# Performance work log

Hardware: AMD Instinct MI355X
Metric: run time of the kernel (lower is better)

## Reference

```python
import jax, jax.numpy as jnp
import numpy as np

B, S, V, D = 8, 1024, 8192, 256
MAX_POS = 1024


def _positional_encoding(position, d_model):
    pos = np.arange(position)[:, None].astype(np.float32)
    i = np.arange(d_model)[None, :].astype(np.float32)
    angle_rads = pos / np.power(10000.0, 2.0 * np.floor(i / 2.0) / np.float32(d_model))
    angle_rads[:, 0::2] = np.sin(angle_rads[:, 0::2])
    angle_rads[:, 1::2] = np.cos(angle_rads[:, 1::2])
    return jnp.asarray(angle_rads[None, ...], dtype=jnp.float32)  # [1, position, d_model]


def setup_inputs() -> dict:
    key = jax.random.key(0)
    k1, k2 = jax.random.split(key)
    x = jax.random.randint(k1, (B, S, V), 0, 2, dtype=jnp.int32)  # multi-hot mask
    emb_table = jax.random.normal(k2, (V, D), dtype=jnp.float32) * 0.02
    pos_enc = _positional_encoding(MAX_POS, D)
    return {"x": x, "emb_table": emb_table, "pos_enc": pos_enc}


def reference(x, emb_table, pos_enc):
    # Multi-hot embedding-bag: sum_v x[b,s,v] * emb_table[v,:]  (dense O(V) reduction,
    # faithful to get_emb's full-vocab embed * mask + reduce_sum)
    seq_len = x.shape[1]
    d_model = emb_table.shape[1]
    xf = x.astype(jnp.float32)
    emb = jnp.einsum('bsv,vd->bsd', xf, emb_table)
    emb = emb * jnp.sqrt(jnp.float32(d_model))
    # positional encoding gated by whether the position has any active token
    any_tok = (jnp.sum(x, axis=-1) > 0).astype(jnp.float32)[..., None]  # [B,S,1]
    out = emb + pos_enc[:, :seq_len, :] * any_tok
    # dropout is identity in eval mode; num_layers = 0 -> no encoder layers
    return out
```

## Files before the change

kernel.cpp:

```cpp
#include <hip/hip_runtime.h>


#define M_TOT 8192
#define K_TOT 8192
#define D_DIM 256
#define KSPLIT 8
#define KCHUNK (K_TOT / KSPLIT)
#define BK 32

typedef short  short8  __attribute__((ext_vector_type(8)));
typedef float  floatx4 __attribute__((ext_vector_type(4)));
typedef int    intx4   __attribute__((ext_vector_type(4)));

union S8U { intx4 i; short8 s; };

#define WS_RS_OFF (4u * 1024u * 1024u)

__device__ __forceinline__ unsigned int bf16_rne(float f) {
    unsigned int u = __float_as_uint(f);
    u += 0x7fffu + ((u >> 16) & 1u);
    return u >> 16;
}

__global__ __launch_bounds__(256) void zero_kernel(float* __restrict__ out, int* __restrict__ rs) {
    int b = blockIdx.x;
    if (b < 2048) {
        floatx4 z = {0.f, 0.f, 0.f, 0.f};
        *(floatx4*)(out + ((size_t)b * 256 + threadIdx.x) * 4) = z;
    } else {
        intx4 z = {0, 0, 0, 0};
        *(intx4*)(rs + ((size_t)(b - 2048) * 256 + threadIdx.x) * 4) = z;
    }
}

__global__ __launch_bounds__(256) void prep_kernel(const float* __restrict__ emb,
                                                   unsigned short* __restrict__ wsBf) {
    int gid = blockIdx.x * 256 + threadIdx.x;
    int l  = gid & 63;
    int kb = (gid >> 6) & 255;
    int c  = gid >> 14;
    int d  = c * 16 + (l & 15);
    int v0 = kb * 32 + (l >> 4) * 8;
    const float* src = emb + (size_t)v0 * D_DIM + d;
    intx4 q;
#pragma unroll
    for (int p = 0; p < 4; ++p) {
        unsigned int u0 = bf16_rne(src[(size_t)(2 * p) * D_DIM] * 16.0f);
        unsigned int u1 = bf16_rne(src[(size_t)(2 * p + 1) * D_DIM] * 16.0f);
        q[p] = (int)(u0 | (u1 << 16));
    }
    *(intx4*)(wsBf + (size_t)gid * 8) = q;
}

__global__ __launch_bounds__(256) void gemm_kernel(const int* __restrict__ x,
                                                   const unsigned short* __restrict__ wsBf,
                                                   float* __restrict__ out,
                                                   int* __restrict__ rs) {
    const int m0   = blockIdx.x * 64;
    const int kbeg = blockIdx.y * KCHUNK;
    const int t    = threadIdx.x;
    const int wave = t >> 6, lane = t & 63;
    const int quad = lane >> 4, rl = lane & 15;
    const int n0   = wave * 64;

    floatx4 acc[4][4];
#pragma unroll
    for (int i = 0; i < 4; ++i)
#pragma unroll
        for (int j = 0; j < 4; ++j) acc[i][j] = (floatx4){0.f, 0.f, 0.f, 0.f};

    int rp[4] = {0, 0, 0, 0};

    const int* abase = x + (size_t)(m0 + rl) * K_TOT + kbeg + quad * 8;
    const unsigned short* bbase = wsBf + ((size_t)(n0 >> 4) * 256) * 512 + (size_t)lane * 8;

#pragma unroll 2
    for (int kk = 0; kk < KCHUNK; kk += BK) {
        const int kb = (kbeg + kk) >> 5;

        short8 bf[4];
#pragma unroll
        for (int j = 0; j < 4; ++j)
            bf[j] = ((const S8U*)(bbase + ((size_t)j * 256 + kb) * 512))->s;

        short8 af[4];
#pragma unroll
        for (int i = 0; i < 4; ++i) {
            const int* p = abase + (size_t)(i * 16) * K_TOT + kk;
            intx4 a0 = *(const intx4*)p;
            intx4 a1 = *(const intx4*)(p + 4);
            int p0 = a0[0] | (a0[1] << 16);
            int p1 = a0[2] | (a0[3] << 16);
            int p2 = a1[0] | (a1[1] << 16);
            int p3 = a1[2] | (a1[3] << 16);
            if (wave == 0) rp[i] += p0 + p1 + p2 + p3;
            S8U u;
            u.i[0] = p0 * 0x3F80;
            u.i[1] = p1 * 0x3F80;
            u.i[2] = p2 * 0x3F80;
            u.i[3] = p3 * 0x3F80;
            af[i] = u.s;
        }

#pragma unroll
        for (int i = 0; i < 4; ++i)
#pragma unroll
            for (int j = 0; j < 4; ++j)
                acc[i][j] = __builtin_amdgcn_mfma_f32_16x16x32_bf16(af[i], bf[j], acc[i][j], 0, 0, 0);
    }

    if (wave == 0) {
#pragma unroll
        for (int i = 0; i < 4; ++i) {
            int cnt = (rp[i] & 0xFFFF) + (rp[i] >> 16);
            cnt += __shfl_xor(cnt, 16);
            cnt += __shfl_xor(cnt, 32);
            if (quad == 0) atomicAdd(&rs[m0 + i * 16 + rl], cnt);
        }
    }

#pragma unroll
    for (int i = 0; i < 4; ++i) {
#pragma unroll
        for (int j = 0; j < 4; ++j) {
            int col = n0 + j * 16 + rl;
#pragma unroll
            for (int r = 0; r < 4; ++r) {
                int row = m0 + i * 16 + quad * 4 + r;
                unsafeAtomicAdd(&out[(size_t)row * D_DIM + col], acc[i][j][r]);
            }
        }
    }
}

__global__ __launch_bounds__(256) void epi_kernel(float* __restrict__ out,
                                                  const float* __restrict__ pos,
                                                  const int* __restrict__ rs) {
    int gid  = blockIdx.x * 256 + threadIdx.x;
    int base = gid * 4;
    int row  = base >> 8;
    int col  = base & 255;
    if (rs[row] > 0) {
        int s = row & 1023;
        floatx4 o = *(floatx4*)(out + base);
        floatx4 p = *(const floatx4*)(pos + (size_t)s * D_DIM + col);
        o += p;
        *(floatx4*)(out + base) = o;
    }
}

extern "C" void kernel_launch(void* const* d_in, const int* in_sizes, int n_in,
                              void* d_out, int out_size, void* d_ws, size_t ws_size,
                              hipStream_t stream) {
    const int*   x   = (const int*)d_in[0];
    const float* emb = (const float*)d_in[1];
    const float* pos = (const float*)d_in[2];
    float*       out = (float*)d_out;

    unsigned short* wsBf = (unsigned short*)d_ws;
    int*            rs   = (int*)((char*)d_ws + WS_RS_OFF);

    zero_kernel<<<dim3(2056), dim3(256), 0, stream>>>(out, rs);
    prep_kernel<<<dim3(1024), dim3(256), 0, stream>>>(emb, wsBf);
    gemm_kernel<<<dim3(128, KSPLIT), dim3(256), 0, stream>>>(x, wsBf, out, rs);
    epi_kernel<<<dim3(2048), dim3(256), 0, stream>>>(out, pos, rs);
}
```

Before: 475.4 us.

## Stage A tiles via async LDS loads, replace atomic split-K with partial-buffer reduction

The GEMM now stages the int32 mask tiles into double-buffered, XOR-swizzled LDS using global_load_lds, so the next tile's global load overlaps the current tile's MFMAs. The tile is reshaped to 32 rows by 256 columns with K split 4 ways. Each split writes plain stores to its own partial buffer instead of atomically adding into a zeroed output. A fused reduce kernel then sums the partials, applies the row-count gate and adds the positional encoding, which removes the zero kernel and the float atomics. The cost is 32 MB of extra partial traffic and more re-reads of the B tiles, since each block now covers fewer rows.

```diff
diff --git a/kernel.cpp b/kernel.cpp
--- a/kernel.cpp
+++ b/kernel.cpp
@@ -1,12 +1,15 @@
 #include <hip/hip_runtime.h>
+#include <stdint.h>
 
 
-#define M_TOT 8192
 #define K_TOT 8192
 #define D_DIM 256
-#define KSPLIT 8
+#define KSPLIT 4
 #define KCHUNK (K_TOT / KSPLIT)
-#define BK 32
+#define BK 64
+#define TROWS 32
+#define NTILES (KCHUNK / BK)
+#define PART_STRIDE (8192u * 256u)
 
 typedef short  short8  __attribute__((ext_vector_type(8)));
 typedef float  floatx4 __attribute__((ext_vector_type(4)));
@@ -14,7 +17,8 @@
 
 union S8U { intx4 i; short8 s; };
 
-#define WS_RS_OFF (4u * 1024u * 1024u)
+#define WS_PART_OFF (4u * 1024u * 1024u)
+#define WS_RS_OFF   (36u * 1024u * 1024u)
 
 __device__ __forceinline__ unsigned int bf16_rne(float f) {
     unsigned int u = __float_as_uint(f);
@@ -22,15 +26,10 @@
     return u >> 16;
 }
 
-__global__ __launch_bounds__(256) void zero_kernel(float* __restrict__ out, int* __restrict__ rs) {
-    int b = blockIdx.x;
-    if (b < 2048) {
-        floatx4 z = {0.f, 0.f, 0.f, 0.f};
-        *(floatx4*)(out + ((size_t)b * 256 + threadIdx.x) * 4) = z;
-    } else {
-        intx4 z = {0, 0, 0, 0};
-        *(intx4*)(rs + ((size_t)(b - 2048) * 256 + threadIdx.x) * 4) = z;
-    }
+__device__ __forceinline__ void load_lds16(const int* g, int* l) {
+    __builtin_amdgcn_global_load_lds((const __attribute__((address_space(1))) unsigned int*)g,
+                                     (__attribute__((address_space(3))) unsigned int*)l,
+                                     16, 0, 0);
 }
 
 __global__ __launch_bounds__(256) void prep_kernel(const float* __restrict__ emb,
@@ -54,99 +53,127 @@
 
 __global__ __launch_bounds__(256) void gemm_kernel(const int* __restrict__ x,
                                                    const unsigned short* __restrict__ wsBf,
-                                                   float* __restrict__ out,
-                                                   int* __restrict__ rs) {
-    const int m0   = blockIdx.x * 64;
-    const int kbeg = blockIdx.y * KCHUNK;
+                                                   float* __restrict__ part,
+                                                   int* __restrict__ rsp) {
+    __shared__ int Al[2][2048];
+
+    const int m0   = blockIdx.x * TROWS;
+    const int kidx = blockIdx.y;
+    const int kbeg = kidx * KCHUNK;
     const int t    = threadIdx.x;
     const int wave = t >> 6, lane = t & 63;
     const int quad = lane >> 4, rl = lane & 15;
-    const int n0   = wave * 64;
+    const int sx   = rl & 7;
 
-    floatx4 acc[4][4];
+    const int row0 = t >> 4;
+    const int kof  = (t & 15) ^ (row0 & 7);
+    const int* g0 = x + (size_t)(m0 + row0) * K_TOT + kbeg + kof * 4;
+    const int* g1 = g0 + (size_t)16 * K_TOT;
+
+    floatx4 acc[2][4];
 #pragma unroll
-    for (int i = 0; i < 4; ++i)
+    for (int i = 0; i < 2; ++i)
 #pragma unroll
         for (int j = 0; j < 4; ++j) acc[i][j] = (floatx4){0.f, 0.f, 0.f, 0.f};
+    int rp[2] = {0, 0};
 
-    int rp[4] = {0, 0, 0, 0};
+    const int kbase = kidx * (KCHUNK / 32);
 
-    const int* abase = x + (size_t)(m0 + rl) * K_TOT + kbeg + quad * 8;
-    const unsigned short* bbase = wsBf + ((size_t)(n0 >> 4) * 256) * 512 + (size_t)lane * 8;
+    load_lds16(g0, &Al[0][t * 4]);
+    load_lds16(g1, &Al[0][1024 + t * 4]);
 
-#pragma unroll 2
-    for (int kk = 0; kk < KCHUNK; kk += BK) {
-        const int kb = (kbeg + kk) >> 5;
-
-        short8 bf[4];
-#pragma unroll
-        for (int j = 0; j < 4; ++j)
-            bf[j] = ((const S8U*)(bbase + ((size_t)j * 256 + kb) * 512))->s;
-
-        short8 af[4];
-#pragma unroll
-        for (int i = 0; i < 4; ++i) {
-            const int* p = abase + (size_t)(i * 16) * K_TOT + kk;
-            intx4 a0 = *(const intx4*)p;
-            intx4 a1 = *(const intx4*)(p + 4);
-            int p0 = a0[0] | (a0[1] << 16);
-            int p1 = a0[2] | (a0[3] << 16);
-            int p2 = a1[0] | (a1[1] << 16);
-            int p3 = a1[2] | (a1[3] << 16);
-            if (wave == 0) rp[i] += p0 + p1 + p2 + p3;
-            S8U u;
-            u.i[0] = p0 * 0x3F80;
-            u.i[1] = p1 * 0x3F80;
-            u.i[2] = p2 * 0x3F80;
-            u.i[3] = p3 * 0x3F80;
-            af[i] = u.s;
+    for (int tl = 0; tl < NTILES; ++tl) {
+        __syncthreads();
+        if (tl + 1 < NTILES) {
+            const int* ga = g0 + (tl + 1) * BK;
+            const int* gb = g1 + (tl + 1) * BK;
+            int* dst = &Al[(tl + 1) & 1][0];
+            load_lds16(ga, dst + t * 4);
+            load_lds16(gb, dst + 1024 + t * 4);
         }
+        const int* buf = &Al[tl & 1][0];
 
 #pragma unroll
-        for (int i = 0; i < 4; ++i)
+        for (int s = 0; s < 2; ++s) {
+            const int kb = kbase + tl * 2 + s;
+
+            short8 bf[4];
 #pragma unroll
             for (int j = 0; j < 4; ++j)
-                acc[i][j] = __builtin_amdgcn_mfma_f32_16x16x32_bf16(af[i], bf[j], acc[i][j], 0, 0, 0);
+                bf[j] = ((const S8U*)(wsBf + ((size_t)((wave * 4 + j) * 256 + kb) * 64 + lane) * 8))->s;
+
+            short8 af[2];
+#pragma unroll
+            for (int i = 0; i < 2; ++i) {
+                int ka = (s * 8 + quad * 2) ^ sx;
+                int kc = (s * 8 + quad * 2 + 1) ^ sx;
+                int rowb = (i * 16 + rl) * 16;
+                intx4 v0 = *(const intx4*)(buf + (rowb + ka) * 4);
+                intx4 v1 = *(const intx4*)(buf + (rowb + kc) * 4);
+                int p0 = v0[0] | (v0[1] << 16);
+                int p1 = v0[2] | (v0[3] << 16);
+                int p2 = v1[0] | (v1[1] << 16);
+                int p3 = v1[2] | (v1[3] << 16);
+                if (wave == 0) rp[i] += p0 + p1 + p2 + p3;
+                S8U u;
+                u.i[0] = p0 * 0x3F80;
+                u.i[1] = p1 * 0x3F80;
+                u.i[2] = p2 * 0x3F80;
+                u.i[3] = p3 * 0x3F80;
+                af[i] = u.s;
+            }
+
+#pragma unroll
+            for (int i = 0; i < 2; ++i)
+#pragma unroll
+                for (int j = 0; j < 4; ++j)
+                    acc[i][j] = __builtin_amdgcn_mfma_f32_16x16x32_bf16(af[i], bf[j], acc[i][j], 0, 0, 0);
+        }
     }
 
     if (wave == 0) {
 #pragma unroll
-        for (int i = 0; i < 4; ++i) {
-            int cnt = (rp[i] & 0xFFFF) + (rp[i] >> 16);
+        for (int i = 0; i < 2; ++i) {
+            int cnt = (rp[i] & 0xFFFF) + ((unsigned)rp[i] >> 16);
             cnt += __shfl_xor(cnt, 16);
             cnt += __shfl_xor(cnt, 32);
-            if (quad == 0) atomicAdd(&rs[m0 + i * 16 + rl], cnt);
+            if (quad == 0) rsp[(size_t)kidx * 8192 + m0 + i * 16 + rl] = cnt;
         }
     }
 
+    float* pk = part + (size_t)kidx * PART_STRIDE;
 #pragma unroll
-    for (int i = 0; i < 4; ++i) {
+    for (int i = 0; i < 2; ++i) {
 #pragma unroll
         for (int j = 0; j < 4; ++j) {
-            int col = n0 + j * 16 + rl;
+            int col = wave * 64 + j * 16 + rl;
 #pragma unroll
             for (int r = 0; r < 4; ++r) {
                 int row = m0 + i * 16 + quad * 4 + r;
-                unsafeAtomicAdd(&out[(size_t)row * D_DIM + col], acc[i][j][r]);
+                pk[(size_t)row * D_DIM + col] = acc[i][j][r];
             }
         }
     }
 }
 
-__global__ __launch_bounds__(256) void epi_kernel(float* __restrict__ out,
-                                                  const float* __restrict__ pos,
-                                                  const int* __restrict__ rs) {
-    int gid  = blockIdx.x * 256 + threadIdx.x;
-    int base = gid * 4;
-    int row  = base >> 8;
-    int col  = base & 255;
-    if (rs[row] > 0) {
+__global__ __launch_bounds__(256) void reduce_kernel(const float* __restrict__ part,
+                                                     const int* __restrict__ rsp,
+                                                     const float* __restrict__ pos,
+                                                     float* __restrict__ out) {
+    int gid = blockIdx.x * 256 + threadIdx.x;
+    size_t base = (size_t)gid * 4;
+    int row = gid >> 6;
+    floatx4 a = *(const floatx4*)(part + base);
+    a += *(const floatx4*)(part + 1 * (size_t)PART_STRIDE + base);
+    a += *(const floatx4*)(part + 2 * (size_t)PART_STRIDE + base);
+    a += *(const floatx4*)(part + 3 * (size_t)PART_STRIDE + base);
+    int rsum = rsp[row] + rsp[8192 + row] + rsp[16384 + row] + rsp[24576 + row];
+    if (rsum > 0) {
         int s = row & 1023;
-        floatx4 o = *(floatx4*)(out + base);
-        floatx4 p = *(const floatx4*)(pos + (size_t)s * D_DIM + col);
-        o += p;
-        *(floatx4*)(out + base) = o;
+        int col = (gid & 63) * 4;
+        a += *(const floatx4*)(pos + (size_t)s * D_DIM + col);
     }
+    *(floatx4*)(out + base) = a;
 }
 
 extern "C" void kernel_launch(void* const* d_in, const int* in_sizes, int n_in,
@@ -158,10 +185,10 @@
     float*       out = (float*)d_out;
 
     unsigned short* wsBf = (unsigned short*)d_ws;
-    int*            rs   = (int*)((char*)d_ws + WS_RS_OFF);
+    float*          part = (float*)((char*)d_ws + WS_PART_OFF);
+    int*            rsp  = (int*)((char*)d_ws + WS_RS_OFF);
 
-    zero_kernel<<<dim3(2056), dim3(256), 0, stream>>>(out, rs);
     prep_kernel<<<dim3(1024), dim3(256), 0, stream>>>(emb, wsBf);
-    gemm_kernel<<<dim3(128, KSPLIT), dim3(256), 0, stream>>>(x, wsBf, out, rs);
-    epi_kernel<<<dim3(2048), dim3(256), 0, stream>>>(out, pos, rs);
+    gemm_kernel<<<dim3(256, KSPLIT), dim3(256), 0, stream>>>(x, wsBf, part, rsp);
+    reduce_kernel<<<dim3(2048), dim3(256), 0, stream>>>(part, rsp, pos, out);
 }
```

Result: faster. 421.7 us (-11.3%).
